# Performance work log

Measured on AMD Instinct MI355X. Metric: run time of the kernel, lower is better.

Reference implementation:

```python
import jax, jax.numpy as jnp
import numpy as np

B, S, D, H = 4, 2048, 1024, 16
DH = D // H  # head dim = 64

def setup_inputs() -> dict:
    key = jax.random.key(0)
    ks = jax.random.split(key, 11)
    sc = 0.02
    return {
        "Q": jax.random.normal(ks[0], (B, S, D), jnp.float32),
        "K": jax.random.normal(ks[1], (B, S, D), jnp.float32),
        "V": jax.random.normal(ks[2], (B, S, D), jnp.float32),
        "Wq": jax.random.normal(ks[3], (D, D), jnp.float32) * sc,
        "bq": jnp.zeros((D,), jnp.float32),
        "Wk": jax.random.normal(ks[4], (D, D), jnp.float32) * sc,
        "bk": jnp.zeros((D,), jnp.float32),
        "Wv": jax.random.normal(ks[5], (D, D), jnp.float32) * sc,
        "bv": jnp.zeros((D,), jnp.float32),
        "Wo": jax.random.normal(ks[6], (D, D), jnp.float32) * sc,
        "bo": jnp.zeros((D,), jnp.float32),
    }

def reference(Q, K, V, Wq, bq, Wk, bk, Wv, bv, Wo, bo):
    # Linear projections (torch nn.Linear: x @ W.T + b)
    def proj(x, W, b):
        y = x @ W.T + b                      # [B,S,D]
        return y.reshape(B, -1, H, DH).transpose(0, 2, 1, 3)  # [B,H,S,DH]
    q = proj(Q, Wq, bq)
    k = proj(K, Wk, bk)
    v = proj(V, Wv, bv)
    scores = jnp.einsum('bhqd,bhkd->bhqk', q, k) / jnp.sqrt(jnp.float32(DH))
    attn = jax.nn.softmax(scores, axis=-1)   # dropout p=0 -> identity
    ctx = jnp.einsum('bhqk,bhkd->bhqd', attn, v)
    ctx = ctx.transpose(0, 2, 1, 3).reshape(B, -1, D)
    return ctx @ Wo.T + bo
```

## Files before the change

kernel.cpp:

```cpp
#include <hip/hip_runtime.h>
#include <hip/hip_bf16.h>
#include <cmath>

constexpr int kB = 4;
constexpr int kS = 2048;
constexpr int kD = 1024;
constexpr int kH = 16;

typedef __attribute__((ext_vector_type(8))) short bf16x8;
typedef __attribute__((ext_vector_type(4))) short bf16x4;
typedef __attribute__((ext_vector_type(4))) float f32x4;
typedef __attribute__((ext_vector_type(4))) unsigned int u32x4;

__device__ __forceinline__ unsigned short f2bf(float f) {
  unsigned int u = __builtin_bit_cast(unsigned int, f);
  u = (u + 0x7fffu + ((u >> 16) & 1u)) >> 16;
  return (unsigned short)u;
}

__device__ __forceinline__ f32x4 mfma16(bf16x8 a, bf16x8 b, f32x4 c) {
  return __builtin_amdgcn_mfma_f32_16x16x32_bf16(a, b, c, 0, 0, 0);
}

#define GL16(gsrc, ldst)                                                      \
  __builtin_amdgcn_global_load_lds(                                           \
      (const __attribute__((address_space(1))) unsigned int*)(gsrc),          \
      (__attribute__((address_space(3))) unsigned int*)(ldst), 16, 0, 0)

#define CVTPK(dst, lo, hi)                                                    \
  asm("v_cvt_pk_bf16_f32 %0, %1, %2" : "=v"(dst) : "v"(lo), "v"(hi))

__global__ __launch_bounds__(256) void cvt_w(
    const float* __restrict__ w0, const float* __restrict__ w1,
    const float* __restrict__ w2, const float* __restrict__ w3,
    unsigned short* __restrict__ o0, unsigned short* __restrict__ o1,
    unsigned short* __restrict__ o2, unsigned short* __restrict__ o3) {
  const float* src = blockIdx.y == 0 ? w0 : blockIdx.y == 1 ? w1
                   : blockIdx.y == 2 ? w2 : w3;
  unsigned short* dst = blockIdx.y == 0 ? o0 : blockIdx.y == 1 ? o1
                      : blockIdx.y == 2 ? o2 : o3;
  const int i = (blockIdx.x * 256 + threadIdx.x) * 8;
  float4 a = *reinterpret_cast<const float4*>(src + i);
  float4 b = *reinterpret_cast<const float4*>(src + i + 4);
  bf16x8 v;
  v[0] = (short)f2bf(a.x); v[1] = (short)f2bf(a.y);
  v[2] = (short)f2bf(a.z); v[3] = (short)f2bf(a.w);
  v[4] = (short)f2bf(b.x); v[5] = (short)f2bf(b.y);
  v[6] = (short)f2bf(b.z); v[7] = (short)f2bf(b.w);
  *reinterpret_cast<bf16x8*>(dst + i) = v;
}

__global__ __launch_bounds__(256, 3) void proj_gemm3(
    const float* __restrict__ Xq, const float* __restrict__ Xk,
    const float* __restrict__ Xv,
    const unsigned short* __restrict__ Wq, const unsigned short* __restrict__ Wk,
    const unsigned short* __restrict__ Wv,
    const float* __restrict__ bq, const float* __restrict__ bk,
    const float* __restrict__ bv,
    unsigned short* __restrict__ oq, unsigned short* __restrict__ ok,
    unsigned short* __restrict__ ov) {
  const int vmode = blockIdx.z;
  const float* X = vmode == 0 ? Xq : vmode == 1 ? Xk : Xv;
  const unsigned short* Wb = vmode == 0 ? Wq : vmode == 1 ? Wk : Wv;
  const float* bias = vmode == 0 ? bq : vmode == 1 ? bk : bv;
  unsigned short* out = vmode == 0 ? oq : vmode == 1 ? ok : ov;
  const float scale = vmode == 0 ? 0.18033688f : 1.0f;

  __shared__ float Af[2][128 * 32];
  __shared__ short Bt[2][128 * 32];
  const int tid = threadIdx.x;
  const int lane = tid & 63;
  const int w = tid >> 6;
  const int wr = w >> 1, wc = w & 1;
  const int lg = lane >> 4, lc = lane & 15;
  const long bm = (long)blockIdx.x * 128;
  const long bn = (long)blockIdx.y * 128;
  const int sw = lc & 7;

  auto stage = [&](int bset, int k0) {
#pragma unroll
    for (int it = 0; it < 4; ++it) {
      const int cb = it * 256 + w * 64;
      const int c = cb + lane;
      const int row = c >> 3, ch = c & 7;
      GL16(X + (bm + row) * kD + k0 + ((ch ^ (row & 7)) << 2), &Af[bset][cb * 4]);
    }
#pragma unroll
    for (int it = 0; it < 2; ++it) {
      const int cb = it * 256 + w * 64;
      const int c = cb + lane;
      const int row = c >> 2, ch = c & 3;
      GL16(Wb + (bn + row) * kD + k0 + (ch << 3), &Bt[bset][cb * 8]);
    }
  };

  f32x4 acc[4][4] = {};
  stage(0, 0);
  __syncthreads();
  int cur = 0;

  for (int ks = 0; ks < 32; ++ks) {
    if (ks + 1 < 32) stage(cur ^ 1, (ks + 1) * 32);
    const float* Ac = &Af[cur][0];
    const short* Bc = &Bt[cur][0];

    bf16x8 af[4], bfr[4];
#pragma unroll
    for (int mi = 0; mi < 4; ++mi) {
      const int row = wr * 64 + mi * 16 + lc;
      f32x4 a0 = *reinterpret_cast<const f32x4*>(Ac + row * 32 + (((lg * 2) ^ sw) << 2));
      f32x4 a1 = *reinterpret_cast<const f32x4*>(Ac + row * 32 + (((lg * 2 + 1) ^ sw) << 2));
      unsigned u0, u1, u2, u3;
      CVTPK(u0, a0[0], a0[1]); CVTPK(u1, a0[2], a0[3]);
      CVTPK(u2, a1[0], a1[1]); CVTPK(u3, a1[2], a1[3]);
      u32x4 uu = {u0, u1, u2, u3};
      af[mi] = __builtin_bit_cast(bf16x8, uu);
    }
#pragma unroll
    for (int ni = 0; ni < 4; ++ni)
      bfr[ni] = *reinterpret_cast<const bf16x8*>(Bc + (wc * 64 + ni * 16 + lc) * 32 + lg * 8);
#pragma unroll
    for (int mi = 0; mi < 4; ++mi)
#pragma unroll
      for (int ni = 0; ni < 4; ++ni)
        acc[mi][ni] = mfma16(af[mi], bfr[ni], acc[mi][ni]);
    __syncthreads();
    cur ^= 1;
  }

#pragma unroll
  for (int mi = 0; mi < 4; ++mi) {
#pragma unroll
    for (int ni = 0; ni < 4; ++ni) {
      const int n = (int)bn + wc * 64 + ni * 16 + lc;
      const float bv = bias[n];
      const int h = n >> 6, dh = n & 63;
#pragma unroll
      for (int i = 0; i < 4; ++i) {
        const int m = (int)bm + wr * 64 + mi * 16 + lg * 4 + i;
        const int b = m >> 11, s = m & 2047;
        const float v = (acc[mi][ni][i] + bv) * scale;
        size_t idx;
        if (vmode == 2)
          idx = ((size_t)((b * kH + h) * 256 + (s >> 3))) * 512 + (size_t)dh * 8 + (s & 7);
        else if (vmode == 1)
          idx = ((size_t)((b * kH + h) * kS + s)) * 64 +
                (((dh >> 3) ^ ((s & 3) | (((s >> 3) & 1) << 2))) << 3) + (dh & 7);
        else
          idx = ((size_t)((b * kH + h) * kS + s)) * 64 + dh;
        out[idx] = f2bf(v);
      }
    }
  }
}

__global__ __launch_bounds__(256, 4) void attn_fwd(
    const unsigned short* __restrict__ qh,
    const unsigned short* __restrict__ khs,
    const unsigned short* __restrict__ vs,
    unsigned short* __restrict__ ctx) {
  __shared__ short Kb[2][4096];
  __shared__ short Vb[2][4096];

  const int tid = threadIdx.x;
  const int lane = tid & 63;
  const int w = tid >> 6;
  const int lg = lane >> 4, lc = lane & 15;
  const int bid = blockIdx.x;
  const int wg = (bid & 7) * 128 + (bid >> 3);
  const int qt = wg & 15;
  const int bh = wg >> 4;
  const int q0w = qt * 128 + w * 32;
  const size_t base = (size_t)bh * kS * 64;
  const int krl = 8 * (lc >> 2) + (lc & 3);
  const int kc = (lg ^ ((lc & 3) | (((lc >> 2) & 1) << 2))) << 3;

  const bf16x8 qa00 = *reinterpret_cast<const bf16x8*>(qh + base + (size_t)(q0w + lc) * 64 + lg * 8);
  const bf16x8 qa01 = *reinterpret_cast<const bf16x8*>(qh + base + (size_t)(q0w + lc) * 64 + 32 + lg * 8);
  const bf16x8 qa10 = *reinterpret_cast<const bf16x8*>(qh + base + (size_t)(q0w + 16 + lc) * 64 + lg * 8);
  const bf16x8 qa11 = *reinterpret_cast<const bf16x8*>(qh + base + (size_t)(q0w + 16 + lc) * 64 + 32 + lg * 8);

  f32x4 o0[4] = {}, o1[4] = {};
  float m0 = -INFINITY, l0 = 0.f;
  float m1 = -INFINITY, l1 = 0.f;

  auto stage = [&](int bset, int kv0) {
#pragma unroll
    for (int it = 0; it < 2; ++it) {
      const int cb = it * 256 + w * 64;
      GL16(khs + base + (size_t)kv0 * 64 + (size_t)(cb + lane) * 8, &Kb[bset][cb * 8]);
      GL16(vs + base + (size_t)kv0 * 64 + (size_t)(cb + lane) * 8, &Vb[bset][cb * 8]);
    }
  };

  stage(0, 0);
  __syncthreads();
  int cur = 0;

  for (int t = 0; t < 32; ++t) {
    if (t + 1 < 32) stage(cur ^ 1, (t + 1) * 64);
    const short* Kc = &Kb[cur][0];
    const short* Vc = &Vb[cur][0];

#pragma unroll
    for (int kv32 = 0; kv32 < 64; kv32 += 32) {
      f32x4 s00, s01, s10, s11;
      __builtin_amdgcn_s_setprio(1);
      {
        const short* kr = Kc + (kv32 + krl) * 64;
        bf16x8 ka = *reinterpret_cast<const bf16x8*>(kr + kc);
        bf16x8 kb = *reinterpret_cast<const bf16x8*>(kr + (kc ^ 32));
        f32x4 z0 = {}, z1 = {};
        z0 = mfma16(ka, qa00, z0); z0 = mfma16(kb, qa01, z0);
        z1 = mfma16(ka, qa10, z1); z1 = mfma16(kb, qa11, z1);
        s00 = z0; s10 = z1;
      }
      {
        const short* kr = Kc + (kv32 + krl + 4) * 64;
        bf16x8 ka = *reinterpret_cast<const bf16x8*>(kr + kc);
        bf16x8 kb = *reinterpret_cast<const bf16x8*>(kr + (kc ^ 32));
        f32x4 z0 = {}, z1 = {};
        z0 = mfma16(ka, qa00, z0); z0 = mfma16(kb, qa01, z0);
        z1 = mfma16(ka, qa10, z1); z1 = mfma16(kb, qa11, z1);
        s01 = z0; s11 = z1;
      }
      __builtin_amdgcn_s_setprio(0);

      bf16x8 pa0, pa1;
      {
        float cm = fmaxf(fmaxf(fmaxf(s00[0], s00[1]), fmaxf(s00[2], s00[3])),
                         fmaxf(fmaxf(s01[0], s01[1]), fmaxf(s01[2], s01[3])));
        cm = fmaxf(cm, __shfl_xor(cm, 16));
        cm = fmaxf(cm, __shfl_xor(cm, 32));
        if (__any(cm > m0 + 11.0f)) {
          float mn = fmaxf(m0, cm);
          float sc = __builtin_amdgcn_exp2f(m0 - mn);
          m0 = mn; l0 *= sc;
#pragma unroll
          for (int i = 0; i < 4; ++i) {
            float si = __shfl(sc, lg * 4 + i);
            o0[0][i] *= si; o0[1][i] *= si; o0[2][i] *= si; o0[3][i] *= si;
          }
        }
        float pA = __builtin_amdgcn_exp2f(s00[0] - m0);
        float pB = __builtin_amdgcn_exp2f(s00[1] - m0);
        float pC = __builtin_amdgcn_exp2f(s00[2] - m0);
        float pD = __builtin_amdgcn_exp2f(s00[3] - m0);
        float pE = __builtin_amdgcn_exp2f(s01[0] - m0);
        float pF = __builtin_amdgcn_exp2f(s01[1] - m0);
        float pG = __builtin_amdgcn_exp2f(s01[2] - m0);
        float pH = __builtin_amdgcn_exp2f(s01[3] - m0);
        float rs = ((pA + pB) + (pC + pD)) + ((pE + pF) + (pG + pH));
        rs += __shfl_xor(rs, 16);
        rs += __shfl_xor(rs, 32);
        l0 += rs;
        unsigned uA, uB, uC, uD;
        CVTPK(uA, pA, pB); CVTPK(uB, pC, pD);
        CVTPK(uC, pE, pF); CVTPK(uD, pG, pH);
        u32x4 uu = {uA, uB, uC, uD};
        pa0 = __builtin_bit_cast(bf16x8, uu);
      }
      {
        float cm = fmaxf(fmaxf(fmaxf(s10[0], s10[1]), fmaxf(s10[2], s10[3])),
                         fmaxf(fmaxf(s11[0], s11[1]), fmaxf(s11[2], s11[3])));
        cm = fmaxf(cm, __shfl_xor(cm, 16));
        cm = fmaxf(cm, __shfl_xor(cm, 32));
        if (__any(cm > m1 + 11.0f)) {
          float mn = fmaxf(m1, cm);
          float sc = __builtin_amdgcn_exp2f(m1 - mn);
          m1 = mn; l1 *= sc;
#pragma unroll
          for (int i = 0; i < 4; ++i) {
            float si = __shfl(sc, lg * 4 + i);
            o1[0][i] *= si; o1[1][i] *= si; o1[2][i] *= si; o1[3][i] *= si;
          }
        }
        float pA = __builtin_amdgcn_exp2f(s10[0] - m1);
        float pB = __builtin_amdgcn_exp2f(s10[1] - m1);
        float pC = __builtin_amdgcn_exp2f(s10[2] - m1);
        float pD = __builtin_amdgcn_exp2f(s10[3] - m1);
        float pE = __builtin_amdgcn_exp2f(s11[0] - m1);
        float pF = __builtin_amdgcn_exp2f(s11[1] - m1);
        float pG = __builtin_amdgcn_exp2f(s11[2] - m1);
        float pH = __builtin_amdgcn_exp2f(s11[3] - m1);
        float rs = ((pA + pB) + (pC + pD)) + ((pE + pF) + (pG + pH));
        rs += __shfl_xor(rs, 16);
        rs += __shfl_xor(rs, 32);
        l1 += rs;
        unsigned uA, uB, uC, uD;
        CVTPK(uA, pA, pB); CVTPK(uB, pC, pD);
        CVTPK(uC, pE, pF); CVTPK(uD, pG, pH);
        u32x4 uu = {uA, uB, uC, uD};
        pa1 = __builtin_bit_cast(bf16x8, uu);
      }

      __builtin_amdgcn_s_setprio(1);
#pragma unroll
      for (int f = 0; f < 4; ++f) {
        bf16x8 vb = *reinterpret_cast<const bf16x8*>(
            Vc + ((kv32 >> 3) + lg) * 512 + (f * 16 + lc) * 8);
        o0[f] = mfma16(pa0, vb, o0[f]);
        o1[f] = mfma16(pa1, vb, o1[f]);
      }
      __builtin_amdgcn_s_setprio(0);
    }
    __syncthreads();
    cur ^= 1;
  }

  const int b = bh >> 4, h = bh & 15;
#pragma unroll
  for (int i = 0; i < 4; ++i) {
    const float inv0 = 1.0f / __shfl(l0, lg * 4 + i);
    const float inv1 = 1.0f / __shfl(l1, lg * 4 + i);
    const int r0 = q0w + lg * 4 + i;
    const int r1 = q0w + 16 + lg * 4 + i;
#pragma unroll
    for (int f = 0; f < 4; ++f) {
      ctx[((size_t)(b * kS + r0)) * kD + h * 64 + f * 16 + lc] = f2bf(o0[f][i] * inv0);
      ctx[((size_t)(b * kS + r1)) * kD + h * 64 + f * 16 + lc] = f2bf(o1[f][i] * inv1);
    }
  }
}

__global__ __launch_bounds__(256, 3) void oproj_gemm2(
    const unsigned short* __restrict__ A, const unsigned short* __restrict__ Wb,
    const float* __restrict__ bias, float* __restrict__ out) {
  __shared__ short At[2][4096];
  __shared__ short Bt[2][4096];
  const int tid = threadIdx.x;
  const int lane = tid & 63;
  const int w = tid >> 6;
  const int wr = w >> 1, wc = w & 1;
  const int lg = lane >> 4, lc = lane & 15;
  const long bm = (long)blockIdx.x * 128;
  const long bn = (long)blockIdx.y * 128;

  auto stage = [&](int bset, int k0) {
#pragma unroll
    for (int it = 0; it < 2; ++it) {
      const int cb = it * 256 + w * 64;
      const int c = cb + lane;
      const int row = c >> 2, seg = c & 3;
      GL16(A + (bm + row) * kD + k0 + seg * 8, &At[bset][cb * 8]);
      GL16(Wb + (bn + row) * kD + k0 + seg * 8, &Bt[bset][cb * 8]);
    }
  };

  f32x4 acc[4][4] = {};
  stage(0, 0);
  __syncthreads();
  int cur = 0;

  for (int ks = 0; ks < 32; ++ks) {
    if (ks + 1 < 32) stage(cur ^ 1, (ks + 1) * 32);
    const short* Ac = &At[cur][0];
    const short* Bc = &Bt[cur][0];
    bf16x8 af[4], bfr[4];
#pragma unroll
    for (int mi = 0; mi < 4; ++mi)
      af[mi] = *reinterpret_cast<const bf16x8*>(Ac + (wr * 64 + mi * 16 + lc) * 32 + lg * 8);
#pragma unroll
    for (int ni = 0; ni < 4; ++ni)
      bfr[ni] = *reinterpret_cast<const bf16x8*>(Bc + (wc * 64 + ni * 16 + lc) * 32 + lg * 8);
#pragma unroll
    for (int mi = 0; mi < 4; ++mi)
#pragma unroll
      for (int ni = 0; ni < 4; ++ni)
        acc[mi][ni] = mfma16(af[mi], bfr[ni], acc[mi][ni]);
    __syncthreads();
    cur ^= 1;
  }

#pragma unroll
  for (int mi = 0; mi < 4; ++mi) {
#pragma unroll
    for (int ni = 0; ni < 4; ++ni) {
      const int n = (int)bn + wc * 64 + ni * 16 + lc;
      const float bv = bias[n];
#pragma unroll
      for (int i = 0; i < 4; ++i) {
        const long m = bm + wr * 64 + mi * 16 + lg * 4 + i;
        out[(size_t)m * kD + n] = acc[mi][ni][i] + bv;
      }
    }
  }
}

extern "C" void kernel_launch(void* const* d_in, const int* in_sizes, int n_in,
                              void* d_out, int out_size, void* d_ws, size_t ws_size,
                              hipStream_t stream) {
  const float* Q  = (const float*)d_in[0];
  const float* K  = (const float*)d_in[1];
  const float* V  = (const float*)d_in[2];
  const float* Wq = (const float*)d_in[3];
  const float* bq = (const float*)d_in[4];
  const float* Wk = (const float*)d_in[5];
  const float* bk = (const float*)d_in[6];
  const float* Wv = (const float*)d_in[7];
  const float* bv = (const float*)d_in[8];
  const float* Wo = (const float*)d_in[9];
  const float* bo = (const float*)d_in[10];
  float* out = (float*)d_out;

  const size_t n_tok = (size_t)kB * kS * kD;
  const size_t n_w = (size_t)kD * kD;
  unsigned short* qh  = (unsigned short*)d_ws;
  unsigned short* kh  = qh + n_tok;
  unsigned short* vsw = kh + n_tok;
  unsigned short* cx  = vsw + n_tok;
  unsigned short* wqb = cx + n_tok;
  unsigned short* wkb = wqb + n_w;
  unsigned short* wvb = wkb + n_w;
  unsigned short* wob = wvb + n_w;

  dim3 blk(256, 1, 1);
  cvt_w<<<dim3(512, 4, 1), blk, 0, stream>>>(Wq, Wk, Wv, Wo, wqb, wkb, wvb, wob);
  proj_gemm3<<<dim3(64, 8, 3), blk, 0, stream>>>(Q, K, V, wqb, wkb, wvb,
                                                 bq, bk, bv, qh, kh, vsw);
  attn_fwd<<<dim3(1024, 1, 1), blk, 0, stream>>>(qh, kh, vsw, cx);
  oproj_gemm2<<<dim3(64, 8, 1), blk, 0, stream>>>(cx, wob, bo, out);
}
```

Measured before the change: 215.6 us.

## Triple-buffer GEMM k-loop and pre-tile weights and context into LDS-ready layout

The projection and output GEMMs move from double to triple buffering, issuing global-to-LDS loads two k-steps ahead and waiting on vmcnt with raw barriers instead of a full __syncthreads. MFMA sections run at raised priority. The weight conversion kernel and the attention epilogue now write bf16 data in a k-chunk-major tiled layout, so each GEMM stage is one contiguous copy and LDS fragment reads are conflict-free. The aim is to hide load latency and cut LDS bank conflicts. The cost is more LDS per block, lower occupancy for proj_gemm3 (launch bound lowered from 3 to 2), and scattered 2-byte stores in the attention epilogue.

```diff
diff --git a/kernel.cpp b/kernel.cpp
--- a/kernel.cpp
+++ b/kernel.cpp
@@ -8,7 +8,6 @@
 constexpr int kH = 16;
 
 typedef __attribute__((ext_vector_type(8))) short bf16x8;
-typedef __attribute__((ext_vector_type(4))) short bf16x4;
 typedef __attribute__((ext_vector_type(4))) float f32x4;
 typedef __attribute__((ext_vector_type(4))) unsigned int u32x4;
 
@@ -29,28 +28,50 @@
 
 #define CVTPK(dst, lo, hi)                                                    \
   asm("v_cvt_pk_bf16_f32 %0, %1, %2" : "=v"(dst) : "v"(lo), "v"(hi))
+
+#define WAITV(n) asm volatile("s_waitcnt vmcnt(" #n ")" ::: "memory")
 
 __global__ __launch_bounds__(256) void cvt_w(
     const float* __restrict__ w0, const float* __restrict__ w1,
     const float* __restrict__ w2, const float* __restrict__ w3,
     unsigned short* __restrict__ o0, unsigned short* __restrict__ o1,
     unsigned short* __restrict__ o2, unsigned short* __restrict__ o3) {
+  __shared__ short Ls[8192];
   const float* src = blockIdx.y == 0 ? w0 : blockIdx.y == 1 ? w1
                    : blockIdx.y == 2 ? w2 : w3;
   unsigned short* dst = blockIdx.y == 0 ? o0 : blockIdx.y == 1 ? o1
                       : blockIdx.y == 2 ? o2 : o3;
-  const int i = (blockIdx.x * 256 + threadIdx.x) * 8;
-  float4 a = *reinterpret_cast<const float4*>(src + i);
-  float4 b = *reinterpret_cast<const float4*>(src + i + 4);
-  bf16x8 v;
-  v[0] = (short)f2bf(a.x); v[1] = (short)f2bf(a.y);
-  v[2] = (short)f2bf(a.z); v[3] = (short)f2bf(a.w);
-  v[4] = (short)f2bf(b.x); v[5] = (short)f2bf(b.y);
-  v[6] = (short)f2bf(b.z); v[7] = (short)f2bf(b.w);
-  *reinterpret_cast<bf16x8*>(dst + i) = v;
-}
-
-__global__ __launch_bounds__(256, 3) void proj_gemm3(
+  const int pn = blockIdx.x >> 4;
+  const int t64 = blockIdx.x & 15;
+  const int tid = threadIdx.x;
+
+#pragma unroll
+  for (int it = 0; it < 4; ++it) {
+    const int u = it * 256 + tid;
+    const int row = u >> 3, k8 = u & 7;
+    const float* s = src + (size_t)(pn * 128 + row) * kD + t64 * 64 + k8 * 8;
+    float4 a = *reinterpret_cast<const float4*>(s);
+    float4 b = *reinterpret_cast<const float4*>(s + 4);
+    bf16x8 v;
+    v[0] = (short)f2bf(a.x); v[1] = (short)f2bf(a.y);
+    v[2] = (short)f2bf(a.z); v[3] = (short)f2bf(a.w);
+    v[4] = (short)f2bf(b.x); v[5] = (short)f2bf(b.y);
+    v[6] = (short)f2bf(b.z); v[7] = (short)f2bf(b.w);
+    *reinterpret_cast<bf16x8*>(&Ls[(k8 * 128 + (row ^ k8)) * 8]) = v;
+  }
+  __syncthreads();
+#pragma unroll
+  for (int it = 0; it < 4; ++it) {
+    const int g = it * 256 + tid;
+    const int ks8 = g >> 7, row = g & 127;
+    bf16x8 v = *reinterpret_cast<const bf16x8*>(&Ls[(ks8 * 128 + (row ^ ks8)) * 8]);
+    const size_t cg = (size_t)pn * 16384 + (size_t)(t64 * 2 + (ks8 >> 2)) * 512 +
+                      (ks8 & 3) * 128 + row;
+    *reinterpret_cast<bf16x8*>(dst + cg * 8) = v;
+  }
+}
+
+__global__ __launch_bounds__(256, 2) void proj_gemm3(
     const float* __restrict__ Xq, const float* __restrict__ Xk,
     const float* __restrict__ Xv,
     const unsigned short* __restrict__ Wq, const unsigned short* __restrict__ Wk,
@@ -66,18 +87,20 @@
   unsigned short* out = vmode == 0 ? oq : vmode == 1 ? ok : ov;
   const float scale = vmode == 0 ? 0.18033688f : 1.0f;
 
-  __shared__ float Af[2][128 * 32];
-  __shared__ short Bt[2][128 * 32];
+  __shared__ float Af[3][128 * 32];
+  __shared__ short Bt[3][128 * 32];
   const int tid = threadIdx.x;
   const int lane = tid & 63;
   const int w = tid >> 6;
   const int wr = w >> 1, wc = w & 1;
   const int lg = lane >> 4, lc = lane & 15;
   const long bm = (long)blockIdx.x * 128;
-  const long bn = (long)blockIdx.y * 128;
+  const int pn = blockIdx.y;
+  const long bn = (long)pn * 128;
   const int sw = lc & 7;
 
-  auto stage = [&](int bset, int k0) {
+  auto stage = [&](int bset, int ks) {
+    const int k0 = ks * 32;
 #pragma unroll
     for (int it = 0; it < 4; ++it) {
       const int cb = it * 256 + w * 64;
@@ -88,19 +111,24 @@
 #pragma unroll
     for (int it = 0; it < 2; ++it) {
       const int cb = it * 256 + w * 64;
-      const int c = cb + lane;
-      const int row = c >> 2, ch = c & 3;
-      GL16(Wb + (bn + row) * kD + k0 + (ch << 3), &Bt[bset][cb * 8]);
+      GL16(Wb + ((size_t)pn * 16384 + (size_t)ks * 512 + cb + lane) * 8,
+           &Bt[bset][cb * 8]);
     }
   };
 
   f32x4 acc[4][4] = {};
   stage(0, 0);
-  __syncthreads();
+  stage(1, 1);
+  WAITV(6);
+  __builtin_amdgcn_s_barrier();
+  __builtin_amdgcn_sched_barrier(0);
   int cur = 0;
 
   for (int ks = 0; ks < 32; ++ks) {
-    if (ks + 1 < 32) stage(cur ^ 1, (ks + 1) * 32);
+    if (ks + 2 < 32) {
+      int b2 = cur + 2; if (b2 >= 3) b2 -= 3;
+      stage(b2, ks + 2);
+    }
     const float* Ac = &Af[cur][0];
     const short* Bc = &Bt[cur][0];
 
@@ -118,14 +146,22 @@
     }
 #pragma unroll
     for (int ni = 0; ni < 4; ++ni)
-      bfr[ni] = *reinterpret_cast<const bf16x8*>(Bc + (wc * 64 + ni * 16 + lc) * 32 + lg * 8);
+      bfr[ni] = *reinterpret_cast<const bf16x8*>(
+          Bc + (lg * 128 + wc * 64 + ni * 16 + lc) * 8);
+    __builtin_amdgcn_s_setprio(1);
 #pragma unroll
     for (int mi = 0; mi < 4; ++mi)
 #pragma unroll
       for (int ni = 0; ni < 4; ++ni)
         acc[mi][ni] = mfma16(af[mi], bfr[ni], acc[mi][ni]);
-    __syncthreads();
-    cur ^= 1;
+    __builtin_amdgcn_s_setprio(0);
+
+    if (ks < 31) {
+      if (ks + 2 < 32) WAITV(6); else WAITV(0);
+      __builtin_amdgcn_s_barrier();
+      __builtin_amdgcn_sched_barrier(0);
+    }
+    cur = cur + 1 == 3 ? 0 : cur + 1;
   }
 
 #pragma unroll
@@ -313,12 +349,16 @@
   for (int i = 0; i < 4; ++i) {
     const float inv0 = 1.0f / __shfl(l0, lg * 4 + i);
     const float inv1 = 1.0f / __shfl(l1, lg * 4 + i);
-    const int r0 = q0w + lg * 4 + i;
-    const int r1 = q0w + 16 + lg * 4 + i;
+    const int m0g = b * kS + q0w + lg * 4 + i;
+    const int m1g = m0g + 16;
 #pragma unroll
     for (int f = 0; f < 4; ++f) {
-      ctx[((size_t)(b * kS + r0)) * kD + h * 64 + f * 16 + lc] = f2bf(o0[f][i] * inv0);
-      ctx[((size_t)(b * kS + r1)) * kD + h * 64 + f * 16 + lc] = f2bf(o1[f][i] * inv1);
+      const int d = h * 64 + f * 16 + lc;
+      const size_t coff = (size_t)(d >> 5) * 512 + ((d >> 3) & 3) * 128;
+      ctx[((size_t)(m0g >> 7) * 16384 + coff + (m0g & 127)) * 8 + (d & 7)] =
+          f2bf(o0[f][i] * inv0);
+      ctx[((size_t)(m1g >> 7) * 16384 + coff + (m1g & 127)) * 8 + (d & 7)] =
+          f2bf(o1[f][i] * inv1);
     }
   }
 }
@@ -326,50 +366,65 @@
 __global__ __launch_bounds__(256, 3) void oproj_gemm2(
     const unsigned short* __restrict__ A, const unsigned short* __restrict__ Wb,
     const float* __restrict__ bias, float* __restrict__ out) {
-  __shared__ short At[2][4096];
-  __shared__ short Bt[2][4096];
+  __shared__ short At[3][4096];
+  __shared__ short Bt[3][4096];
   const int tid = threadIdx.x;
   const int lane = tid & 63;
   const int w = tid >> 6;
   const int wr = w >> 1, wc = w & 1;
   const int lg = lane >> 4, lc = lane & 15;
-  const long bm = (long)blockIdx.x * 128;
-  const long bn = (long)blockIdx.y * 128;
-
-  auto stage = [&](int bset, int k0) {
+  const int pm = blockIdx.x;
+  const int pn = blockIdx.y;
+  const long bm = (long)pm * 128;
+  const long bn = (long)pn * 128;
+
+  auto stage = [&](int bset, int ks) {
 #pragma unroll
     for (int it = 0; it < 2; ++it) {
       const int cb = it * 256 + w * 64;
-      const int c = cb + lane;
-      const int row = c >> 2, seg = c & 3;
-      GL16(A + (bm + row) * kD + k0 + seg * 8, &At[bset][cb * 8]);
-      GL16(Wb + (bn + row) * kD + k0 + seg * 8, &Bt[bset][cb * 8]);
+      GL16(A + ((size_t)pm * 16384 + (size_t)ks * 512 + cb + lane) * 8,
+           &At[bset][cb * 8]);
+      GL16(Wb + ((size_t)pn * 16384 + (size_t)ks * 512 + cb + lane) * 8,
+           &Bt[bset][cb * 8]);
     }
   };
 
   f32x4 acc[4][4] = {};
   stage(0, 0);
-  __syncthreads();
+  stage(1, 1);
+  WAITV(4);
+  __builtin_amdgcn_s_barrier();
+  __builtin_amdgcn_sched_barrier(0);
   int cur = 0;
 
   for (int ks = 0; ks < 32; ++ks) {
-    if (ks + 1 < 32) stage(cur ^ 1, (ks + 1) * 32);
+    if (ks + 2 < 32) {
+      int b2 = cur + 2; if (b2 >= 3) b2 -= 3;
+      stage(b2, ks + 2);
+    }
     const short* Ac = &At[cur][0];
     const short* Bc = &Bt[cur][0];
     bf16x8 af[4], bfr[4];
 #pragma unroll
     for (int mi = 0; mi < 4; ++mi)
-      af[mi] = *reinterpret_cast<const bf16x8*>(Ac + (wr * 64 + mi * 16 + lc) * 32 + lg * 8);
+      af[mi] = *reinterpret_cast<const bf16x8*>(Ac + (lg * 128 + wr * 64 + mi * 16 + lc) * 8);
 #pragma unroll
     for (int ni = 0; ni < 4; ++ni)
-      bfr[ni] = *reinterpret_cast<const bf16x8*>(Bc + (wc * 64 + ni * 16 + lc) * 32 + lg * 8);
+      bfr[ni] = *reinterpret_cast<const bf16x8*>(Bc + (lg * 128 + wc * 64 + ni * 16 + lc) * 8);
+    __builtin_amdgcn_s_setprio(1);
 #pragma unroll
     for (int mi = 0; mi < 4; ++mi)
 #pragma unroll
       for (int ni = 0; ni < 4; ++ni)
         acc[mi][ni] = mfma16(af[mi], bfr[ni], acc[mi][ni]);
-    __syncthreads();
-    cur ^= 1;
+    __builtin_amdgcn_s_setprio(0);
+
+    if (ks < 31) {
+      if (ks + 2 < 32) WAITV(4); else WAITV(0);
+      __builtin_amdgcn_s_barrier();
+      __builtin_amdgcn_sched_barrier(0);
+    }
+    cur = cur + 1 == 3 ? 0 : cur + 1;
   }
 
 #pragma unroll
@@ -415,7 +470,7 @@
   unsigned short* wob = wvb + n_w;
 
   dim3 blk(256, 1, 1);
-  cvt_w<<<dim3(512, 4, 1), blk, 0, stream>>>(Wq, Wk, Wv, Wo, wqb, wkb, wvb, wob);
+  cvt_w<<<dim3(128, 4, 1), blk, 0, stream>>>(Wq, Wk, Wv, Wo, wqb, wkb, wvb, wob);
   proj_gemm3<<<dim3(64, 8, 3), blk, 0, stream>>>(Q, K, V, wqb, wkb, wvb,
                                                  bq, bk, bv, qh, kh, vsw);
   attn_fwd<<<dim3(1024, 1, 1), blk, 0, stream>>>(qh, kh, vsw, cx);
```

Measured after the change: 232.4 us. 1.08x slower.
